# Kernel optimization log

Measured on AMD Instinct MI355X. Metric: run time of the kernel, lower is better.

## Reference

```python
import jax, jax.numpy as jnp
import numpy as np

ALPHA = 0.999  # decay_alpha (<= 1.0 branch of stream_inference)
BH, TQ, S, D = 128, 1, 8192, 64  # (batch*heads, query len, kv window, head dim)


def setup_inputs() -> dict:
    key = jax.random.key(0)
    ks = jax.random.split(key, 6)
    return {
        "q": jax.random.normal(ks[0], (BH, TQ, D), jnp.float32),
        "k": jax.random.normal(ks[1], (BH, S, D), jnp.float32),
        "v": jax.random.normal(ks[2], (BH, S, D), jnp.float32),
        "q_push": jax.random.normal(ks[3], (BH, TQ, D), jnp.float32),
        "k_push": jax.random.normal(ks[4], (BH, 1, D), jnp.float32),
        "v_push": jax.random.normal(ks[5], (BH, 1, D), jnp.float32),
        "attn_mask": jnp.zeros((BH, TQ, S), jnp.float32),
    }


def reference(q, k, v, q_push, k_push, v_push, attn_mask):
    """Faithful DotProductAttentionStream.stream_inference (alpha <= 1.0 path):
    cold-start cache build followed by one streaming push step with decay.
    Returns the output after the push step ([BH, TQ, D])."""
    # ---- cold start: build QK_exp / QKV_exp / Z caches ----
    QK = jnp.einsum("btd,bsd->bts", q, k)                     # [BH,TQ,S]
    QK_max = jnp.max(QK, axis=-1, keepdims=True)              # running max (frozen)
    QK_exp = jnp.exp(QK - QK_max + attn_mask)                 # [BH,TQ,S]
    QKV_exp = jnp.einsum("bts,bsd->btd", QK_exp, v)           # [BH,TQ,D]
    Z = jnp.sum(QK_exp, axis=-1, keepdims=True)               # [BH,TQ,1]
    # (cold-start output would be QKV_exp / Z)

    # ---- push step: incremental update with exponential decay ----
    QK_push = jnp.einsum("btd,bnd->btn", q_push, k_push)      # [BH,TQ,1]
    QK_exp_push = jnp.exp(QK_push - QK_max)                   # reuse frozen running max
    sum_push = jnp.sum(QK_exp_push, axis=-1, keepdims=True)
    QKV_exp_push = jnp.einsum("btn,bnd->btd", QK_exp_push, v_push)
    QKV_exp_new = ALPHA * QKV_exp + QKV_exp_push
    Z_new = ALPHA * Z + sum_push
    return QKV_exp_new / Z_new
```

## Files before the change

kernel.cpp:

```cpp
#include <hip/hip_runtime.h>
#include <math.h>

#define BH 128
#define S  8192
#define D  64
#define ALPHA_F 0.999f

#define CHUNK   1024
#define NCHUNK  (S / CHUNK)
#define PSTRIDE 72

__global__ __launch_bounds__(256) void partial_kernel(
    const float* __restrict__ q,
    const float* __restrict__ k,
    const float* __restrict__ v,
    const float* __restrict__ mask,
    float* __restrict__ ws)
{
    const int blk   = blockIdx.x;
    const int bh    = blk / NCHUNK;
    const int chunk = blk % NCHUNK;
    const int s0    = chunk * CHUNK;
    const int t     = threadIdx.x;
    const int lid   = t & 15;
    const int g     = t >> 4;
    const int wave  = t >> 6;

    __shared__ float sc[CHUNK];
    __shared__ float red[8];
    __shared__ float o_parts[16][64];

    const float4 q4 = *reinterpret_cast<const float4*>(q + bh * D + lid * 4);

    const float* kb = k + (size_t)bh * S * D;
    const float* vb = v + (size_t)bh * S * D;
    const float* mb = mask + (size_t)bh * S;

    float lmax = -INFINITY;
    #pragma unroll 4
    for (int it = 0; it < CHUNK / 16; ++it) {
        const int sl = it * 16 + g;
        const int s  = s0 + sl;
        const float4 k4 = *reinterpret_cast<const float4*>(kb + (size_t)s * D + lid * 4);
        float d = q4.x * k4.x + q4.y * k4.y + q4.z * k4.z + q4.w * k4.w;
        d += __shfl_xor(d, 1);
        d += __shfl_xor(d, 2);
        d += __shfl_xor(d, 4);
        d += __shfl_xor(d, 8);
        d += mb[s];
        if (lid == 0) sc[sl] = d;
        lmax = fmaxf(lmax, d);
    }

    #pragma unroll
    for (int off = 1; off < 64; off <<= 1) lmax = fmaxf(lmax, __shfl_xor(lmax, off));
    if ((t & 63) == 0) red[wave] = lmax;
    __syncthreads();
    const float M = fmaxf(fmaxf(red[0], red[1]), fmaxf(red[2], red[3]));

    float zl = 0.f;
    #pragma unroll
    for (int s = t; s < CHUNK; s += 256) {
        const float p = __expf(sc[s] - M);
        sc[s] = p;
        zl += p;
    }
    #pragma unroll
    for (int off = 1; off < 64; off <<= 1) zl += __shfl_xor(zl, off);
    if ((t & 63) == 0) red[4 + wave] = zl;
    __syncthreads();

    const int dq = t & 15;
    const int sr = t >> 4;
    float4 o4 = {0.f, 0.f, 0.f, 0.f};
    #pragma unroll 4
    for (int it = 0; it < CHUNK / 16; ++it) {
        const int sl = it * 16 + sr;
        const float p = sc[sl];
        const float4 v4 = *reinterpret_cast<const float4*>(vb + (size_t)(s0 + sl) * D + dq * 4);
        o4.x += p * v4.x;
        o4.y += p * v4.y;
        o4.z += p * v4.z;
        o4.w += p * v4.w;
    }
    o_parts[sr][dq * 4 + 0] = o4.x;
    o_parts[sr][dq * 4 + 1] = o4.y;
    o_parts[sr][dq * 4 + 2] = o4.z;
    o_parts[sr][dq * 4 + 3] = o4.w;
    __syncthreads();

    if (t < 64) {
        float acc = 0.f;
        #pragma unroll
        for (int r = 0; r < 16; ++r) acc += o_parts[r][t];
        float* rec = ws + (size_t)blk * PSTRIDE;
        rec[4 + t] = acc;
        if (t == 0) {
            rec[0] = M;
            rec[1] = red[4] + red[5] + red[6] + red[7];
        }
    }
}

__global__ __launch_bounds__(64) void reduce_kernel(
    const float* __restrict__ q_push,
    const float* __restrict__ k_push,
    const float* __restrict__ v_push,
    const float* __restrict__ ws,
    float* __restrict__ out)
{
    const int bh = blockIdx.x;
    const int t  = threadIdx.x;
    const float* base = ws + (size_t)bh * NCHUNK * PSTRIDE;

    float M = -INFINITY;
    #pragma unroll
    for (int c = 0; c < NCHUNK; ++c) M = fmaxf(M, base[c * PSTRIDE]);

    float z = 0.f, o = 0.f;
    #pragma unroll
    for (int c = 0; c < NCHUNK; ++c) {
        const float w = __expf(base[c * PSTRIDE] - M);
        z += w * base[c * PSTRIDE + 1];
        o += w * base[c * PSTRIDE + 4 + t];
    }

    float pd = q_push[bh * D + t] * k_push[bh * D + t];
    #pragma unroll
    for (int off = 1; off < 64; off <<= 1) pd += __shfl_xor(pd, off);
    const float p = __expf(pd - M);

    out[bh * D + t] = (ALPHA_F * o + p * v_push[bh * D + t]) / (ALPHA_F * z + p);
}

extern "C" void kernel_launch(void* const* d_in, const int* in_sizes, int n_in,
                              void* d_out, int out_size, void* d_ws, size_t ws_size,
                              hipStream_t stream) {
    const float* q      = (const float*)d_in[0];
    const float* k      = (const float*)d_in[1];
    const float* v      = (const float*)d_in[2];
    const float* q_push = (const float*)d_in[3];
    const float* k_push = (const float*)d_in[4];
    const float* v_push = (const float*)d_in[5];
    const float* mask   = (const float*)d_in[6];
    float* ws  = (float*)d_ws;
    float* out = (float*)d_out;

    partial_kernel<<<dim3(BH * NCHUNK), dim3(256), 0, stream>>>(q, k, v, mask, ws);
    reduce_kernel<<<dim3(BH), dim3(64), 0, stream>>>(q_push, k_push, v_push, ws, out);
}
```

Baseline: 510.9 us.

## Fuse score and PV passes via per-group online softmax, halve chunk size

Replaces the three-phase chunk kernel (scores to LDS, block max/exp/sum, then a separate V pass) with a single loop. Each 16-lane group keeps a running max, denominator and output accumulator, loading K and V rows together, and the groups are merged in LDS at the end. Chunk size drops to 512, which doubles the block count to improve occupancy and latency hiding. The cost is two exps per row per lane, redundant across the 16 lanes of a group, plus a serial rescale dependency. The reduce kernel now merges twice as many partial records.

```diff
diff --git a/kernel.cpp b/kernel.cpp
--- a/kernel.cpp
+++ b/kernel.cpp
@@ -6,7 +6,7 @@
 #define D  64
 #define ALPHA_F 0.999f
 
-#define CHUNK   1024
+#define CHUNK   512
 #define NCHUNK  (S / CHUNK)
 #define PSTRIDE 72
 
@@ -24,11 +24,10 @@
     const int t     = threadIdx.x;
     const int lid   = t & 15;
     const int g     = t >> 4;
-    const int wave  = t >> 6;
 
-    __shared__ float sc[CHUNK];
-    __shared__ float red[8];
-    __shared__ float o_parts[16][64];
+    __shared__ float gm[16];
+    __shared__ float gz[16];
+    __shared__ float go[16][64];
 
     const float4 q4 = *reinterpret_cast<const float4*>(q + bh * D + lid * 4);
 
@@ -36,69 +35,56 @@
     const float* vb = v + (size_t)bh * S * D;
     const float* mb = mask + (size_t)bh * S;
 
-    float lmax = -INFINITY;
+    float  m  = -INFINITY;
+    float  z  = 0.f;
+    float4 o4 = {0.f, 0.f, 0.f, 0.f};
+
     #pragma unroll 4
     for (int it = 0; it < CHUNK / 16; ++it) {
         const int sl = it * 16 + g;
         const int s  = s0 + sl;
         const float4 k4 = *reinterpret_cast<const float4*>(kb + (size_t)s * D + lid * 4);
+        const float4 v4 = *reinterpret_cast<const float4*>(vb + (size_t)s * D + lid * 4);
+
         float d = q4.x * k4.x + q4.y * k4.y + q4.z * k4.z + q4.w * k4.w;
         d += __shfl_xor(d, 1);
         d += __shfl_xor(d, 2);
         d += __shfl_xor(d, 4);
         d += __shfl_xor(d, 8);
         d += mb[s];
-        if (lid == 0) sc[sl] = d;
-        lmax = fmaxf(lmax, d);
+
+        const float mn = fmaxf(m, d);
+        const float c  = __expf(m - mn);
+        const float p  = __expf(d - mn);
+        z    = z * c + p;
+        o4.x = o4.x * c + p * v4.x;
+        o4.y = o4.y * c + p * v4.y;
+        o4.z = o4.z * c + p * v4.z;
+        o4.w = o4.w * c + p * v4.w;
+        m    = mn;
     }
 
-    #pragma unroll
-    for (int off = 1; off < 64; off <<= 1) lmax = fmaxf(lmax, __shfl_xor(lmax, off));
-    if ((t & 63) == 0) red[wave] = lmax;
-    __syncthreads();
-    const float M = fmaxf(fmaxf(red[0], red[1]), fmaxf(red[2], red[3]));
-
-    float zl = 0.f;
-    #pragma unroll
-    for (int s = t; s < CHUNK; s += 256) {
-        const float p = __expf(sc[s] - M);
-        sc[s] = p;
-        zl += p;
-    }
-    #pragma unroll
-    for (int off = 1; off < 64; off <<= 1) zl += __shfl_xor(zl, off);
-    if ((t & 63) == 0) red[4 + wave] = zl;
-    __syncthreads();
-
-    const int dq = t & 15;
-    const int sr = t >> 4;
-    float4 o4 = {0.f, 0.f, 0.f, 0.f};
-    #pragma unroll 4
-    for (int it = 0; it < CHUNK / 16; ++it) {
-        const int sl = it * 16 + sr;
-        const float p = sc[sl];
-        const float4 v4 = *reinterpret_cast<const float4*>(vb + (size_t)(s0 + sl) * D + dq * 4);
-        o4.x += p * v4.x;
-        o4.y += p * v4.y;
-        o4.z += p * v4.z;
-        o4.w += p * v4.w;
-    }
-    o_parts[sr][dq * 4 + 0] = o4.x;
-    o_parts[sr][dq * 4 + 1] = o4.y;
-    o_parts[sr][dq * 4 + 2] = o4.z;
-    o_parts[sr][dq * 4 + 3] = o4.w;
+    go[g][lid * 4 + 0] = o4.x;
+    go[g][lid * 4 + 1] = o4.y;
+    go[g][lid * 4 + 2] = o4.z;
+    go[g][lid * 4 + 3] = o4.w;
+    if (lid == 0) { gm[g] = m; gz[g] = z; }
     __syncthreads();
 
     if (t < 64) {
-        float acc = 0.f;
+        float M = -INFINITY;
         #pragma unroll
-        for (int r = 0; r < 16; ++r) acc += o_parts[r][t];
+        for (int c2 = 0; c2 < 16; ++c2) M = fmaxf(M, gm[c2]);
+        float zz = 0.f, oo = 0.f;
+        #pragma unroll
+        for (int c2 = 0; c2 < 16; ++c2) {
+            const float w = __expf(gm[c2] - M);
+            zz += w * gz[c2];
+            oo += w * go[c2][t];
+        }
         float* rec = ws + (size_t)blk * PSTRIDE;
-        rec[4 + t] = acc;
-        if (t == 0) {
-            rec[0] = M;
-            rec[1] = red[4] + red[5] + red[6] + red[7];
-        }
+        rec[4 + t] = oo;
+        if (t == 0) { rec[0] = M; rec[1] = zz; }
     }
 }
 
```

Result: no change. 516.2 us (+1.0%).
